# Kernel tuning notes

Hardware: AMD Instinct MI355X
Metric: run time of the kernel (lower is better)

Reference implementation:

```python
import jax, jax.numpy as jnp
import numpy as np

NUM_HEADS = 16
NUM_KV_HEADS = 4
HEAD_DIM = 128
HIDDEN = 2048
SEQ = 2048
BATCH = 2
Q_PER_GROUP = NUM_HEADS // NUM_KV_HEADS          # 4
GROUP_SIZE = (Q_PER_GROUP + 2) * HEAD_DIM        # 768
TOTAL_PROJ = NUM_KV_HEADS * GROUP_SIZE           # 3072


def setup_inputs() -> dict:
    key = jax.random.key(0)
    k1, k2, k3 = jax.random.split(key, 3)
    x = jax.random.normal(k1, (SEQ, BATCH, HIDDEN), dtype=jnp.float32)
    w_qkv = jax.random.normal(k2, (TOTAL_PROJ, HIDDEN), dtype=jnp.float32) * 0.02
    w_proj = jax.random.normal(k3, (HIDDEN, NUM_HEADS * HEAD_DIM), dtype=jnp.float32) * 0.02
    return {"x": x, "w_qkv": w_qkv, "w_proj": w_proj}


def reference(x, w_qkv, w_proj):
    s, b, _ = x.shape
    # fused QKV projection (GQA-packed layout: per kv-group [q...q, k, v])
    qkv = jnp.einsum('sbh,ph->sbp', x, w_qkv)                       # [s,b,3072]
    qkv = qkv.reshape(s, b, NUM_KV_HEADS, GROUP_SIZE)
    q = qkv[..., :Q_PER_GROUP * HEAD_DIM].reshape(s, b, NUM_HEADS, HEAD_DIM)
    k = qkv[..., Q_PER_GROUP * HEAD_DIM:(Q_PER_GROUP + 1) * HEAD_DIM]  # [s,b,kvh,d]
    v = qkv[..., (Q_PER_GROUP + 1) * HEAD_DIM:]                        # [s,b,kvh,d]
    # to [b, heads, s, d]; expand kv heads over query groups (GQA)
    q = q.transpose(1, 2, 0, 3)
    k = jnp.repeat(k.transpose(1, 2, 0, 3), Q_PER_GROUP, axis=1)
    v = jnp.repeat(v.transpose(1, 2, 0, 3), Q_PER_GROUP, axis=1)
    scale = 1.0 / jnp.sqrt(jnp.asarray(HEAD_DIM, dtype=x.dtype))
    scores = jnp.einsum('bhsd,bhtd->bhst', q, k) * scale           # [b,h,s,s]
    attn = jax.nn.softmax(scores, axis=-1)
    out = jnp.einsum('bhst,bhtd->bhsd', attn, v)                    # [b,h,s,d]
    out = out.transpose(2, 0, 1, 3).reshape(s, b, NUM_HEADS * HEAD_DIM)
    return jnp.einsum('sbe,he->sbh', out, w_proj)                   # [s,b,hidden]
```

## Files before the change

### kernel.cpp

```cpp
#include <hip/hip_runtime.h>
#include <hip/hip_bf16.h>

typedef __bf16 bf16;
typedef __bf16 bf16x8 __attribute__((ext_vector_type(8)));
typedef __bf16 bf16x4v __attribute__((ext_vector_type(4)));
typedef float  f32x4  __attribute__((ext_vector_type(4)));
typedef float  f32x16 __attribute__((ext_vector_type(16)));

#define SEQL  2048
#define BATCH 2
#define HID   2048
#define NH    16
#define NKVH  4
#define HD    128
#define NPROJ 3072
#define MROWS 4096

#define QSCALE (0.08838834764831845f * 1.44269504088896340f)

__device__ __forceinline__ void gload16(const void* src, void* dst) {
  __builtin_amdgcn_global_load_lds(
      (__attribute__((address_space(1))) void*)src,
      (__attribute__((address_space(3))) void*)dst, 16, 0, 0);
}

__device__ __forceinline__ int swz128(int off) { return off ^ (((off >> 7) & 7) << 4); }
__device__ __forceinline__ int swz256(int off) { return off ^ (((off >> 8) & 7) << 4); }

__device__ __forceinline__ unsigned cvtpk_bf16(float lo, float hi) {
  unsigned r;
  asm("v_cvt_pk_bf16_f32 %0, %1, %2" : "=v"(r) : "v"(lo), "v"(hi));
  return r;
}
__device__ __forceinline__ void permswap32(unsigned& a, unsigned& b) {
  asm volatile("v_permlane32_swap_b32 %0, %1" : "+v"(a), "+v"(b));
}
__device__ __forceinline__ f32x16 mfma16(bf16x8 a, bf16x8 b, f32x16 c) {
  return __builtin_amdgcn_mfma_f32_32x32x16_bf16(a, b, c, 0, 0, 0);
}
__device__ __forceinline__ float sum16(const f32x16& v) {
  float a = (v[0] + v[1]) + (v[2] + v[3]);
  float b = (v[4] + v[5]) + (v[6] + v[7]);
  float c = (v[8] + v[9]) + (v[10] + v[11]);
  float d = (v[12] + v[13]) + (v[14] + v[15]);
  return (a + b) + (c + d);
}

__global__ __launch_bounds__(256) void cvt_kernel(
    const float* __restrict__ x, const float* __restrict__ wq, const float* __restrict__ wp,
    bf16* __restrict__ xo, bf16* __restrict__ wqo, bf16* __restrict__ wpo) {
  const int NXQ  = (MROWS * HID) / 4;
  const int NWQQ = (NPROJ * HID) / 4;
  const int NWPQ = (HID * HID) / 4;
  const int total = NXQ + NWQQ + NWPQ;
  for (int i = blockIdx.x * blockDim.x + threadIdx.x; i < total; i += gridDim.x * blockDim.x) {
    const float4* src; bf16* dst; int j;
    if (i < NXQ)            { src = (const float4*)x;  dst = xo;  j = i; }
    else if (i < NXQ + NWQQ){ src = (const float4*)wq; dst = wqo; j = i - NXQ; }
    else                    { src = (const float4*)wp; dst = wpo; j = i - NXQ - NWQQ; }
    float4 v = src[j];
    bf16x4v o;
    o[0] = (bf16)v.x; o[1] = (bf16)v.y; o[2] = (bf16)v.z; o[3] = (bf16)v.w;
    *(bf16x4v*)(dst + (size_t)j * 4) = o;
  }
}

__global__ __launch_bounds__(512) void qkv_gemm(
    const bf16* __restrict__ A, const bf16* __restrict__ B,
    bf16* __restrict__ Qo, bf16* __restrict__ Ko, bf16* __restrict__ Vt) {
  __shared__ char lds[131072];
  const int tid = threadIdx.x, l = tid & 63, w = tid >> 6;
  const int wm = w >> 2, wn = w & 3;
  const int lin = blockIdx.x;
  const int swz = (lin & 7) * 24 + (lin >> 3);
  const int bx = swz % 12, by = swz / 12;
  const int r0 = by * 256, p0 = bx * 256;

  f32x4 acc[8][4];
  const f32x4 fzero = {0.f, 0.f, 0.f, 0.f};
#pragma unroll
  for (int m = 0; m < 8; m++)
#pragma unroll
    for (int n = 0; n < 4; n++) acc[m][n] = fzero;

  int sr[4], sc[4];
#pragma unroll
  for (int q = 0; q < 4; q++) {
    const int doff = (q * 512 + tid) * 16;
    sr[q] = doff >> 7;
    sc[q] = ((((doff >> 4) & 7) ^ (sr[q] & 7)) << 4);
  }

  int aoff[8][2], boff[4][2];
#pragma unroll
  for (int m = 0; m < 8; m++)
#pragma unroll
    for (int kk = 0; kk < 2; kk++)
      aoff[m][kk] = swz128((wm * 128 + m * 16 + (l & 15)) * 128 + kk * 64 + (l >> 4) * 16);
#pragma unroll
  for (int n = 0; n < 4; n++)
#pragma unroll
    for (int kk = 0; kk < 2; kk++)
      boff[n][kk] = swz128((wn * 64 + n * 16 + (l & 15)) * 128 + kk * 64 + (l >> 4) * 16);

  auto stage = [&](int t, int buf) {
    const int k0 = t * 64;
#pragma unroll
    for (int q = 0; q < 4; q++) {
      gload16((const char*)A + ((size_t)(r0 + sr[q]) * HID + k0) * 2 + sc[q],
              lds + buf * 32768 + (q * 512 + (w * 64)) * 16);
      gload16((const char*)B + ((size_t)(p0 + sr[q]) * HID + k0) * 2 + sc[q],
              lds + 65536 + buf * 32768 + (q * 512 + (w * 64)) * 16);
    }
  };

  auto compute = [&](int t) {
    const int bufb = (t & 1) * 32768;
#pragma unroll
    for (int kk = 0; kk < 2; kk++) {
      bf16x8 af[8], bfv[4];
#pragma unroll
      for (int m = 0; m < 8; m++)
        af[m] = *(const bf16x8*)(lds + bufb + aoff[m][kk]);
#pragma unroll
      for (int n = 0; n < 4; n++)
        bfv[n] = *(const bf16x8*)(lds + 65536 + bufb + boff[n][kk]);
#pragma unroll
      for (int m = 0; m < 8; m++)
#pragma unroll
        for (int n = 0; n < 4; n++)
          acc[m][n] = __builtin_amdgcn_mfma_f32_16x16x32_bf16(af[m], bfv[n], acc[m][n], 0, 0, 0);
    }
  };

  stage(0, 0);
  stage(1, 1);
  asm volatile("s_waitcnt vmcnt(8)" ::: "memory");
  __builtin_amdgcn_sched_barrier(0);
  __builtin_amdgcn_s_barrier();
  __builtin_amdgcn_sched_barrier(0);

  for (int t = 0; t < HID / 64; ++t) {
    compute(t);
    __builtin_amdgcn_sched_barrier(0);
    __builtin_amdgcn_s_barrier();
    __builtin_amdgcn_sched_barrier(0);
    if (t + 2 < HID / 64) {
      stage(t + 2, t & 1);
      asm volatile("s_waitcnt vmcnt(8)" ::: "memory");
    } else if (t + 1 < HID / 64) {
      asm volatile("s_waitcnt vmcnt(0)" ::: "memory");
    }
    __builtin_amdgcn_sched_barrier(0);
    __builtin_amdgcn_s_barrier();
    __builtin_amdgcn_sched_barrier(0);
  }

#pragma unroll
  for (int m = 0; m < 8; m++) {
    const int rbase = r0 + wm * 128 + m * 16 + ((l >> 4) << 2);
#pragma unroll
    for (int n = 0; n < 4; n++) {
      const int pc = p0 + wn * 64 + n * 16;
      const int seg = (pc % 768) / 128;
      const int g = pc / 768;
      const int c = (pc % 128) + (l & 15);
#pragma unroll
      for (int rg = 0; rg < 4; ++rg) {
        const int r = rbase + rg;
        const int s = r >> 1, b = r & 1;
        if (seg < 4) {
          const int h = g * 4 + seg;
          Qo[(((size_t)(b * 16 + h)) * 2048 + s) * 128 + c] = (bf16)(acc[m][n][rg] * QSCALE);
        } else if (seg == 4) {
          Ko[(((size_t)(b * 4 + g)) * 2048 + s) * 128 + c] = (bf16)acc[m][n][rg];
        } else {
          Vt[(((size_t)(b * 4 + g)) * 128 + c) * 2048 + s] = (bf16)acc[m][n][rg];
        }
      }
    }
  }
}

template<int BASE>
__device__ __forceinline__ void attn_tile(
    char* lds, const bf16x8* qf, const int* ka, const int* va,
    f32x16* oacc, float& lp) {
  const f32x16 z16 = {};

  f32x16 sT0 = z16, sT1 = z16;
  __builtin_amdgcn_s_setprio(1);
#pragma unroll
  for (int s = 0; s < 8; s++) {
    bf16x8 kf = *(const bf16x8*)(lds + BASE + ka[s]);
    sT0 = mfma16(kf, qf[s], sT0);
  }
#pragma unroll
  for (int s = 0; s < 8; s++) {
    bf16x8 kf = *(const bf16x8*)(lds + BASE + ka[8 + s]);
    sT1 = mfma16(kf, qf[s], sT1);
  }
  __builtin_amdgcn_s_setprio(0);

  unsigned c0[8], c1[8];
#pragma unroll
  for (int i = 0; i < 16; i++) sT0[i] = exp2f(sT0[i]);
  lp += sum16(sT0);
#pragma unroll
  for (int i = 0; i < 8; i++) c0[i] = cvtpk_bf16(sT0[2 * i], sT0[2 * i + 1]);
  permswap32(c0[0], c0[2]); permswap32(c0[1], c0[3]);
  permswap32(c0[4], c0[6]); permswap32(c0[5], c0[7]);

  __builtin_amdgcn_s_setprio(1);
#pragma unroll
  for (int ks = 0; ks < 2; ks++) {
    union { unsigned u[4]; bf16x8 v; } pb;
#pragma unroll
    for (int i = 0; i < 4; i++) pb.u[i] = c0[(ks & 1) * 4 + i];
#pragma unroll
    for (int dblk = 0; dblk < 4; dblk++) {
      bf16x8 vf = *(const bf16x8*)(lds + BASE + 16384 + va[ks * 4 + dblk]);
      oacc[dblk] = mfma16(vf, pb.v, oacc[dblk]);
    }
  }
  __builtin_amdgcn_s_setprio(0);

#pragma unroll
  for (int i = 0; i < 16; i++) sT1[i] = exp2f(sT1[i]);
  lp += sum16(sT1);
#pragma unroll
  for (int i = 0; i < 8; i++) c1[i] = cvtpk_bf16(sT1[2 * i], sT1[2 * i + 1]);
  permswap32(c1[0], c1[2]); permswap32(c1[1], c1[3]);
  permswap32(c1[4], c1[6]); permswap32(c1[5], c1[7]);

  __builtin_amdgcn_s_setprio(1);
#pragma unroll
  for (int ks = 2; ks < 4; ks++) {
    union { unsigned u[4]; bf16x8 v; } pb;
#pragma unroll
    for (int i = 0; i < 4; i++) pb.u[i] = c1[(ks & 1) * 4 + i];
#pragma unroll
    for (int dblk = 0; dblk < 4; dblk++) {
      bf16x8 vf = *(const bf16x8*)(lds + BASE + 16384 + va[ks * 4 + dblk]);
      oacc[dblk] = mfma16(vf, pb.v, oacc[dblk]);
    }
  }
  __builtin_amdgcn_s_setprio(0);
}

__global__ __launch_bounds__(256, 2) void attn_kernel(
    const bf16* __restrict__ Q, const bf16* __restrict__ K, const bf16* __restrict__ V,
    bf16* __restrict__ O) {
  __shared__ char lds[65536];
  const int tid = threadIdx.x, l = tid & 63, w = tid >> 6;
  const int l31 = l & 31, h2 = l >> 5;
  const int lin = blockIdx.x + (blockIdx.y << 4);
  const int swzb = (lin & 7) * 64 + (lin >> 3);
  const int qt = swzb & 15, bh = swzb >> 4;
  const int b = bh >> 4, head = bh & 15, g = head >> 2;

  const int q0 = qt * 128 + w * 32;

  bf16x8 qf[8];
  {
    const bf16* qbase = Q + (((size_t)(b * 16 + head)) * 2048 + q0 + l31) * 128 + h2 * 8;
#pragma unroll
    for (int s = 0; s < 8; s++) qf[s] = *(const bf16x8*)(qbase + s * 16);
  }

  int ka[16], va[16];
#pragma unroll
  for (int tsub = 0; tsub < 2; tsub++)
#pragma unroll
    for (int s = 0; s < 8; s++)
      ka[tsub * 8 + s] = swz256((tsub * 32 + l31) * 256 + s * 32 + h2 * 16);
#pragma unroll
  for (int ks = 0; ks < 4; ks++)
#pragma unroll
    for (int dblk = 0; dblk < 4; dblk++)
      va[ks * 4 + dblk] = swz128((dblk * 32 + l31) * 128 + ks * 32 + h2 * 16);

  int kso[4], vso[4];
#pragma unroll
  for (int q = 0; q < 4; q++) {
    const int off = (q * 4 + w) * 1024 + l * 16;
    kso[q] = swz256(off);
    const int rowv = off >> 7;
    const int chv = ((off >> 4) & 7) ^ (rowv & 7);
    vso[q] = rowv * 4096 + chv * 16;
  }

  const f32x16 z16 = {};
  f32x16 oacc[4];
#pragma unroll
  for (int d = 0; d < 4; d++) oacc[d] = z16;
  float lp = 0.f;

  const char* kbase = (const char*)(K + ((size_t)(b * 4 + g)) * 2048 * 128);
  const char* vbase = (const char*)(V + ((size_t)(b * 4 + g)) * 128 * 2048);

  auto stage = [&](int t0, int B) {
#pragma unroll
    for (int q = 0; q < 4; q++) {
      gload16(kbase + (size_t)t0 * 256 + kso[q], lds + B + (q * 4 + w) * 1024);
      gload16(vbase + (size_t)t0 * 2 + vso[q], lds + B + 16384 + (q * 4 + w) * 1024);
    }
  };

  stage(0, 0);
  __syncthreads();

  for (int t0 = 0; t0 < SEQL; t0 += 128) {
    stage(t0 + 64, 32768);
    attn_tile<0>(lds, qf, ka, va, oacc, lp);
    __syncthreads();
    if (t0 + 128 < SEQL) stage(t0 + 128, 0);
    attn_tile<32768>(lds, qf, ka, va, oacc, lp);
    __syncthreads();
  }

  const float inv = 1.0f / (lp + __shfl_xor(lp, 32));
  const size_t rowo = ((size_t)(q0 + l31) * 2 + b) * 2048 + (size_t)head * 128;
#pragma unroll
  for (int dblk = 0; dblk < 4; dblk++)
#pragma unroll
    for (int g4 = 0; g4 < 4; g4++) {
      bf16x4v ov;
#pragma unroll
      for (int e = 0; e < 4; e++) ov[e] = (bf16)(oacc[dblk][g4 * 4 + e] * inv);
      *(bf16x4v*)(O + rowo + dblk * 32 + g4 * 8 + h2 * 4) = ov;
    }
}

__global__ __launch_bounds__(256, 2) void proj_gemm(
    const bf16* __restrict__ A, const bf16* __restrict__ B, float* __restrict__ C) {
  __shared__ char lds[32768];
  const int tid = threadIdx.x, l = tid & 63, w = tid >> 6;
  const int lin = blockIdx.x + (blockIdx.y << 4);
  const int swz = (lin & 7) * 64 + (lin >> 3);
  const int bx = swz & 15, by = swz >> 4;
  const int r0 = by * 128, p0 = bx * 128;
  const int wr = w >> 1, wc = w & 1;

  f32x4 acc[4][4];
  const f32x4 fzero = {0.f, 0.f, 0.f, 0.f};
#pragma unroll
  for (int m = 0; m < 4; m++)
#pragma unroll
    for (int n = 0; n < 4; n++) acc[m][n] = fzero;

  for (int kt = 0; kt < HID / 64; ++kt) {
    const int k0 = kt * 64;
    __syncthreads();
#pragma unroll
    for (int q = 0; q < 4; q++) {
      const int doff = (w * 4 + q) * 1024 + l * 16;
      const int row = doff >> 7;
      const int chv = ((doff >> 4) & 7) ^ (row & 7);
      gload16((const char*)A + ((size_t)(r0 + row) * HID + k0) * 2 + chv * 16,
              lds + (w * 4 + q) * 1024);
      gload16((const char*)B + ((size_t)(p0 + row) * HID + k0) * 2 + chv * 16,
              lds + 16384 + (w * 4 + q) * 1024);
    }
    __syncthreads();
    bf16x8 af[4][2], bfr[4][2];
#pragma unroll
    for (int m = 0; m < 4; m++)
#pragma unroll
      for (int kk = 0; kk < 2; kk++) {
        int off = (wr * 64 + m * 16 + (l & 15)) * 128 + kk * 64 + (l >> 4) * 16;
        af[m][kk] = *(const bf16x8*)(lds + swz128(off));
      }
#pragma unroll
    for (int n = 0; n < 4; n++)
#pragma unroll
      for (int kk = 0; kk < 2; kk++) {
        int off = (wc * 64 + n * 16 + (l & 15)) * 128 + kk * 64 + (l >> 4) * 16;
        bfr[n][kk] = *(const bf16x8*)(lds + 16384 + swz128(off));
      }
#pragma unroll
    for (int kk = 0; kk < 2; kk++)
#pragma unroll
      for (int m = 0; m < 4; m++)
#pragma unroll
        for (int n = 0; n < 4; n++)
          acc[m][n] = __builtin_amdgcn_mfma_f32_16x16x32_bf16(af[m][kk], bfr[n][kk], acc[m][n], 0, 0, 0);
  }
#pragma unroll
  for (int m = 0; m < 4; m++) {
    const int rbase = r0 + wr * 64 + m * 16 + ((l >> 4) << 2);
#pragma unroll
    for (int n = 0; n < 4; n++) {
      const int c = p0 + wc * 64 + n * 16 + (l & 15);
#pragma unroll
      for (int rg = 0; rg < 4; ++rg)
        C[(size_t)(rbase + rg) * HID + c] = acc[m][n][rg];
    }
  }
}

extern "C" void kernel_launch(void* const* d_in, const int* in_sizes, int n_in,
                              void* d_out, int out_size, void* d_ws, size_t ws_size,
                              hipStream_t stream) {
  const float* x  = (const float*)d_in[0];
  const float* wq = (const float*)d_in[1];
  const float* wp = (const float*)d_in[2];
  float* out = (float*)d_out;
  char* ws = (char*)d_ws;

  size_t off = 0;
  bf16* xb  = (bf16*)(ws + off); off += (size_t)MROWS * HID * 2;
  bf16* wqb = (bf16*)(ws + off); off += (size_t)NPROJ * HID * 2;
  bf16* wpb = (bf16*)(ws + off); off += (size_t)HID * HID * 2;
  bf16* Qb  = (bf16*)(ws + off); off += (size_t)2 * 16 * 2048 * 128 * 2;
  bf16* Kb  = (bf16*)(ws + off); off += (size_t)2 * 4 * 2048 * 128 * 2;
  bf16* Vb  = (bf16*)(ws + off); off += (size_t)2 * 4 * 128 * 2048 * 2;
  bf16* Ob  = xb;

  cvt_kernel<<<2048, 256, 0, stream>>>(x, wq, wp, xb, wqb, wpb);
  qkv_gemm<<<dim3(192), 512, 0, stream>>>(xb, wqb, Qb, Kb, Vb);
  attn_kernel<<<dim3(16, 32), 256, 0, stream>>>(Qb, Kb, Vb, Ob);
  proj_gemm<<<dim3(16, 32), 256, 0, stream>>>(Ob, wpb, out);
}
```

Baseline: 210.9 us.

## Retile QKV and output-projection GEMMs into a shared double-buffered 256-row template

Pulls the double-buffered, direct-to-LDS GEMM mainloop into a template parameterised by the number of N fragments. The QKV GEMM now uses 256x192 tiles over 256 blocks instead of 256x256 over 192 blocks, so the grid matches the 256 CUs of the MI355X. The projection GEMM moves from a single-buffered 128x128 kernel with 256 threads to the pipelined 256x128 kernel with 512 threads. The aim is better CU occupancy and load/compute overlap. The trade-off is smaller N tiles, which mean lower arithmetic intensity per block, plus retuned vmcnt wait counts that must match the new load counts.

```diff
diff --git a/kernel.cpp b/kernel.cpp
--- a/kernel.cpp
+++ b/kernel.cpp
@@ -65,103 +65,122 @@
   }
 }
 
-__global__ __launch_bounds__(512) void qkv_gemm(
-    const bf16* __restrict__ A, const bf16* __restrict__ B,
-    bf16* __restrict__ Qo, bf16* __restrict__ Ko, bf16* __restrict__ Vt) {
-  __shared__ char lds[131072];
-  const int tid = threadIdx.x, l = tid & 63, w = tid >> 6;
+template<int NF, int BSZB>
+__device__ __forceinline__ void gemm_main(
+    const bf16* __restrict__ A, const bf16* __restrict__ Bm,
+    int r0, int p0, char* lds, f32x4 (&acc)[8][NF], int tid, int l, int w) {
   const int wm = w >> 2, wn = w & 3;
-  const int lin = blockIdx.x;
-  const int swz = (lin & 7) * 24 + (lin >> 3);
-  const int bx = swz % 12, by = swz / 12;
-  const int r0 = by * 256, p0 = bx * 256;
-
-  f32x4 acc[8][4];
-  const f32x4 fzero = {0.f, 0.f, 0.f, 0.f};
-#pragma unroll
-  for (int m = 0; m < 8; m++)
-#pragma unroll
-    for (int n = 0; n < 4; n++) acc[m][n] = fzero;
-
-  int sr[4], sc[4];
+
+  int sra[4], sca[4];
 #pragma unroll
   for (int q = 0; q < 4; q++) {
     const int doff = (q * 512 + tid) * 16;
-    sr[q] = doff >> 7;
-    sc[q] = ((((doff >> 4) & 7) ^ (sr[q] & 7)) << 4);
-  }
-
-  int aoff[8][2], boff[4][2];
+    sra[q] = doff >> 7;
+    sca[q] = ((((doff >> 4) & 7) ^ (sra[q] & 7)) << 4);
+  }
+  int srb[NF], scb[NF];
+#pragma unroll
+  for (int q = 0; q < NF; q++) {
+    const int doff = (q * 512 + tid) * 16;
+    srb[q] = doff >> 7;
+    scb[q] = ((((doff >> 4) & 7) ^ (srb[q] & 7)) << 4);
+  }
+
+  int aoff[8][2], boff[NF][2];
 #pragma unroll
   for (int m = 0; m < 8; m++)
 #pragma unroll
     for (int kk = 0; kk < 2; kk++)
       aoff[m][kk] = swz128((wm * 128 + m * 16 + (l & 15)) * 128 + kk * 64 + (l >> 4) * 16);
 #pragma unroll
-  for (int n = 0; n < 4; n++)
+  for (int n = 0; n < NF; n++)
 #pragma unroll
     for (int kk = 0; kk < 2; kk++)
-      boff[n][kk] = swz128((wn * 64 + n * 16 + (l & 15)) * 128 + kk * 64 + (l >> 4) * 16);
+      boff[n][kk] = swz128((wn * (NF * 16) + n * 16 + (l & 15)) * 128 + kk * 64 + (l >> 4) * 16);
 
   auto stage = [&](int t, int buf) {
     const int k0 = t * 64;
 #pragma unroll
-    for (int q = 0; q < 4; q++) {
-      gload16((const char*)A + ((size_t)(r0 + sr[q]) * HID + k0) * 2 + sc[q],
-              lds + buf * 32768 + (q * 512 + (w * 64)) * 16);
-      gload16((const char*)B + ((size_t)(p0 + sr[q]) * HID + k0) * 2 + sc[q],
-              lds + 65536 + buf * 32768 + (q * 512 + (w * 64)) * 16);
-    }
+    for (int q = 0; q < 4; q++)
+      gload16((const char*)A + ((size_t)(r0 + sra[q]) * HID + k0) * 2 + sca[q],
+              lds + buf * 32768 + (q * 512 + w * 64) * 16);
+#pragma unroll
+    for (int q = 0; q < NF; q++)
+      gload16((const char*)Bm + ((size_t)(p0 + srb[q]) * HID + k0) * 2 + scb[q],
+              lds + 65536 + buf * BSZB + (q * 512 + w * 64) * 16);
   };
 
   auto compute = [&](int t) {
-    const int bufb = (t & 1) * 32768;
+    const int ab = (t & 1) * 32768;
+    const int bb = 65536 + (t & 1) * BSZB;
 #pragma unroll
     for (int kk = 0; kk < 2; kk++) {
-      bf16x8 af[8], bfv[4];
+      bf16x8 af[8], bfv[NF];
+#pragma unroll
+      for (int m = 0; m < 8; m++) af[m] = *(const bf16x8*)(lds + ab + aoff[m][kk]);
+#pragma unroll
+      for (int n = 0; n < NF; n++) bfv[n] = *(const bf16x8*)(lds + bb + boff[n][kk]);
 #pragma unroll
       for (int m = 0; m < 8; m++)
-        af[m] = *(const bf16x8*)(lds + bufb + aoff[m][kk]);
-#pragma unroll
-      for (int n = 0; n < 4; n++)
-        bfv[n] = *(const bf16x8*)(lds + 65536 + bufb + boff[n][kk]);
-#pragma unroll
-      for (int m = 0; m < 8; m++)
-#pragma unroll
-        for (int n = 0; n < 4; n++)
+#pragma unroll
+        for (int n = 0; n < NF; n++)
           acc[m][n] = __builtin_amdgcn_mfma_f32_16x16x32_bf16(af[m], bfv[n], acc[m][n], 0, 0, 0);
     }
   };
 
   stage(0, 0);
   stage(1, 1);
-  asm volatile("s_waitcnt vmcnt(8)" ::: "memory");
+  if constexpr (NF == 3) asm volatile("s_waitcnt vmcnt(7)" ::: "memory");
+  else                   asm volatile("s_waitcnt vmcnt(6)" ::: "memory");
   __builtin_amdgcn_sched_barrier(0);
   __builtin_amdgcn_s_barrier();
   __builtin_amdgcn_sched_barrier(0);
 
-  for (int t = 0; t < HID / 64; ++t) {
+  const int NT = HID / 64;
+  for (int t = 0; t < NT; ++t) {
     compute(t);
     __builtin_amdgcn_sched_barrier(0);
     __builtin_amdgcn_s_barrier();
     __builtin_amdgcn_sched_barrier(0);
-    if (t + 2 < HID / 64) {
+    if (t + 2 < NT) {
       stage(t + 2, t & 1);
-      asm volatile("s_waitcnt vmcnt(8)" ::: "memory");
-    } else if (t + 1 < HID / 64) {
+      if constexpr (NF == 3) asm volatile("s_waitcnt vmcnt(7)" ::: "memory");
+      else                   asm volatile("s_waitcnt vmcnt(6)" ::: "memory");
+    } else if (t + 1 < NT) {
       asm volatile("s_waitcnt vmcnt(0)" ::: "memory");
     }
     __builtin_amdgcn_sched_barrier(0);
     __builtin_amdgcn_s_barrier();
     __builtin_amdgcn_sched_barrier(0);
   }
+}
+
+__global__ __launch_bounds__(512) void qkv_gemm(
+    const bf16* __restrict__ A, const bf16* __restrict__ B,
+    bf16* __restrict__ Qo, bf16* __restrict__ Ko, bf16* __restrict__ Vt) {
+  __shared__ char lds[114688];
+  const int tid = threadIdx.x, l = tid & 63, w = tid >> 6;
+  const int wm = w >> 2, wn = w & 3;
+  const int lin = blockIdx.x;
+  const int swz = (lin & 7) * 32 + (lin >> 3);
+  const int bx = swz & 15, by = swz >> 4;
+  const int r0 = by * 256, p0 = bx * 192;
+
+  f32x4 acc[8][3];
+  const f32x4 fzero = {0.f, 0.f, 0.f, 0.f};
+#pragma unroll
+  for (int m = 0; m < 8; m++)
+#pragma unroll
+    for (int n = 0; n < 3; n++) acc[m][n] = fzero;
+
+  gemm_main<3, 24576>(A, B, r0, p0, lds, acc, tid, l, w);
 
 #pragma unroll
   for (int m = 0; m < 8; m++) {
     const int rbase = r0 + wm * 128 + m * 16 + ((l >> 4) << 2);
 #pragma unroll
-    for (int n = 0; n < 4; n++) {
-      const int pc = p0 + wn * 64 + n * 16;
+    for (int n = 0; n < 3; n++) {
+      const int pc = p0 + wn * 48 + n * 16;
       const int seg = (pc % 768) / 128;
       const int g = pc / 768;
       const int c = (pc % 128) + (l & 15);
@@ -182,6 +201,38 @@
   }
 }
 
+__global__ __launch_bounds__(512) void proj_gemm(
+    const bf16* __restrict__ A, const bf16* __restrict__ B, float* __restrict__ C) {
+  __shared__ char lds[98304];
+  const int tid = threadIdx.x, l = tid & 63, w = tid >> 6;
+  const int wm = w >> 2, wn = w & 3;
+  const int lin = blockIdx.x;
+  const int swz = (lin & 7) * 32 + (lin >> 3);
+  const int bx = swz & 15, by = swz >> 4;
+  const int r0 = by * 256, p0 = bx * 128;
+
+  f32x4 acc[8][2];
+  const f32x4 fzero = {0.f, 0.f, 0.f, 0.f};
+#pragma unroll
+  for (int m = 0; m < 8; m++)
+#pragma unroll
+    for (int n = 0; n < 2; n++) acc[m][n] = fzero;
+
+  gemm_main<2, 16384>(A, B, r0, p0, lds, acc, tid, l, w);
+
+#pragma unroll
+  for (int m = 0; m < 8; m++) {
+    const int rbase = r0 + wm * 128 + m * 16 + ((l >> 4) << 2);
+#pragma unroll
+    for (int n = 0; n < 2; n++) {
+      const int c = p0 + wn * 32 + n * 16 + (l & 15);
+#pragma unroll
+      for (int rg = 0; rg < 4; ++rg)
+        C[(size_t)(rbase + rg) * HID + c] = acc[m][n][rg];
+    }
+  }
+}
+
 template<int BASE>
 __device__ __forceinline__ void attn_tile(
     char* lds, const bf16x8* qf, const int* ka, const int* va,
@@ -332,73 +383,6 @@
     }
 }
 
-__global__ __launch_bounds__(256, 2) void proj_gemm(
-    const bf16* __restrict__ A, const bf16* __restrict__ B, float* __restrict__ C) {
-  __shared__ char lds[32768];
-  const int tid = threadIdx.x, l = tid & 63, w = tid >> 6;
-  const int lin = blockIdx.x + (blockIdx.y << 4);
-  const int swz = (lin & 7) * 64 + (lin >> 3);
-  const int bx = swz & 15, by = swz >> 4;
-  const int r0 = by * 128, p0 = bx * 128;
-  const int wr = w >> 1, wc = w & 1;
-
-  f32x4 acc[4][4];
-  const f32x4 fzero = {0.f, 0.f, 0.f, 0.f};
-#pragma unroll
-  for (int m = 0; m < 4; m++)
-#pragma unroll
-    for (int n = 0; n < 4; n++) acc[m][n] = fzero;
-
-  for (int kt = 0; kt < HID / 64; ++kt) {
-    const int k0 = kt * 64;
-    __syncthreads();
-#pragma unroll
-    for (int q = 0; q < 4; q++) {
-      const int doff = (w * 4 + q) * 1024 + l * 16;
-      const int row = doff >> 7;
-      const int chv = ((doff >> 4) & 7) ^ (row & 7);
-      gload16((const char*)A + ((size_t)(r0 + row) * HID + k0) * 2 + chv * 16,
-              lds + (w * 4 + q) * 1024);
-      gload16((const char*)B + ((size_t)(p0 + row) * HID + k0) * 2 + chv * 16,
-              lds + 16384 + (w * 4 + q) * 1024);
-    }
-    __syncthreads();
-    bf16x8 af[4][2], bfr[4][2];
-#pragma unroll
-    for (int m = 0; m < 4; m++)
-#pragma unroll
-      for (int kk = 0; kk < 2; kk++) {
-        int off = (wr * 64 + m * 16 + (l & 15)) * 128 + kk * 64 + (l >> 4) * 16;
-        af[m][kk] = *(const bf16x8*)(lds + swz128(off));
-      }
-#pragma unroll
-    for (int n = 0; n < 4; n++)
-#pragma unroll
-      for (int kk = 0; kk < 2; kk++) {
-        int off = (wc * 64 + n * 16 + (l & 15)) * 128 + kk * 64 + (l >> 4) * 16;
-        bfr[n][kk] = *(const bf16x8*)(lds + 16384 + swz128(off));
-      }
-#pragma unroll
-    for (int kk = 0; kk < 2; kk++)
-#pragma unroll
-      for (int m = 0; m < 4; m++)
-#pragma unroll
-        for (int n = 0; n < 4; n++)
-          acc[m][n] = __builtin_amdgcn_mfma_f32_16x16x32_bf16(af[m][kk], bfr[n][kk], acc[m][n], 0, 0, 0);
-  }
-#pragma unroll
-  for (int m = 0; m < 4; m++) {
-    const int rbase = r0 + wr * 64 + m * 16 + ((l >> 4) << 2);
-#pragma unroll
-    for (int n = 0; n < 4; n++) {
-      const int c = p0 + wc * 64 + n * 16 + (l & 15);
-#pragma unroll
-      for (int rg = 0; rg < 4; ++rg)
-        C[(size_t)(rbase + rg) * HID + c] = acc[m][n][rg];
-    }
-  }
-}
-
 extern "C" void kernel_launch(void* const* d_in, const int* in_sizes, int n_in,
                               void* d_out, int out_size, void* d_ws, size_t ws_size,
                               hipStream_t stream) {
@@ -418,7 +402,7 @@
   bf16* Ob  = xb;
 
   cvt_kernel<<<2048, 256, 0, stream>>>(x, wq, wp, xb, wqb, wpb);
-  qkv_gemm<<<dim3(192), 512, 0, stream>>>(xb, wqb, Qb, Kb, Vb);
+  qkv_gemm<<<dim3(256), 512, 0, stream>>>(xb, wqb, Qb, Kb, Vb);
   attn_kernel<<<dim3(16, 32), 256, 0, stream>>>(Qb, Kb, Vb, Ob);
-  proj_gemm<<<dim3(16, 32), 256, 0, stream>>>(Ob, wpb, out);
-}
+  proj_gemm<<<dim3(256), 512, 0, stream>>>(Ob, wpb, out);
+}
```

Measured after the change: 205.1 us. 2.8% less time.
